# Optimization experiments

Hardware: AMD Instinct MI355X
Metric: run time of the kernel (lower is better)

Reference implementation:

```python
import jax, jax.numpy as jnp
import numpy as np

LN_EPS = 1e-6          # flax nn.LayerNorm default
ATTN_EPS = 1e-9        # numerical_stabilizer default


def ln_points(x, scale, bias):
    """flax LayerNorm(reduction_axes=-2): stats over points axis, affine over feature axis."""
    mu = jnp.mean(x, axis=-2, keepdims=True)
    var = jnp.mean(jnp.square(x), axis=-2, keepdims=True) - jnp.square(mu)
    return (x - mu) * jax.lax.rsqrt(var + LN_EPS) * scale + bias


def self_attention_layer(x, wq_i, bq_i, wk_i, bk_i, wv_i, bv_i, wo_i, bo_i, ls_i, lb_i):
    # 1x1 convs == pointwise linears
    q = x @ wq_i + bq_i                                  # [B,N,C]
    k = x @ wk_i + bk_i
    v = x @ wv_i + bv_i
    attn = jnp.einsum('bmc,bnc->bmn', q, k)              # [B,M,N]
    attn = jax.nn.softmax(attn, axis=-1)
    # extra offset-attention renorm: divide by column sums (axis=1)
    attn = attn / (ATTN_EPS + jnp.sum(attn, axis=1, keepdims=True))
    # einsum '...MN,...NC->...NC' reduces M: scales v by column sums
    col = jnp.sum(attn, axis=1)                          # [B,N]
    out = col[..., None] * v                             # [B,N,C]
    out = out @ wo_i + bo_i
    out = jax.nn.relu(ln_points(out, ls_i, lb_i))
    return out + x


def setup_inputs() -> dict:
    key = jax.random.key(0)
    ks = jax.random.split(key, 16)
    B, N, IN, C, F, L = 2, 4096, 3, 256, 1024, 4
    s_in = 1.0 / np.sqrt(IN)
    s_c = 1.0 / np.sqrt(C)
    s_f = 1.0 / np.sqrt(L * C)
    return {
        'inputs': jax.random.normal(ks[0], (B, N, IN), jnp.float32),
        'w0': jax.random.normal(ks[1], (IN, C), jnp.float32) * s_in,
        'b0': jnp.zeros((C,), jnp.float32),
        'ln0_s': jnp.ones((C,), jnp.float32),
        'ln0_b': jnp.zeros((C,), jnp.float32),
        'w1': jax.random.normal(ks[2], (C, C), jnp.float32) * s_c,
        'b1': jnp.zeros((C,), jnp.float32),
        'ln1_s': jnp.ones((C,), jnp.float32),
        'ln1_b': jnp.zeros((C,), jnp.float32),
        'wq': jax.random.normal(ks[3], (L, C, C), jnp.float32) * s_c,
        'bq': jnp.zeros((L, C), jnp.float32),
        'wk': jax.random.normal(ks[4], (L, C, C), jnp.float32) * s_c,
        'bk': jnp.zeros((L, C), jnp.float32),
        'wv': jax.random.normal(ks[5], (L, C, C), jnp.float32) * s_c,
        'bv': jnp.zeros((L, C), jnp.float32),
        'wo': jax.random.normal(ks[6], (L, C, C), jnp.float32) * s_c,
        'bo': jnp.zeros((L, C), jnp.float32),
        'attn_ln_s': jnp.ones((L, C), jnp.float32),
        'attn_ln_b': jnp.zeros((L, C), jnp.float32),
        'wf': jax.random.normal(ks[7], (L * C, F), jnp.float32) * s_f,
        'bf': jnp.zeros((F,), jnp.float32),
    }


def reference(inputs, w0, b0, ln0_s, ln0_b, w1, b1, ln1_s, ln1_b,
              wq, bq, wk, bk, wv, bv, wo, bo, attn_ln_s, attn_ln_b, wf, bf):
    # pre-conv stack
    out = ln_points(inputs @ w0 + b0, ln0_s, ln0_b)
    out = ln_points(out @ w1 + b1, ln1_s, ln1_b)
    # attention stack (4 structurally identical layers, concatenated)
    attn_outs = []
    for i in range(wq.shape[0]):
        out = self_attention_layer(out, wq[i], bq[i], wk[i], bk[i],
                                   wv[i], bv[i], wo[i], bo[i],
                                   attn_ln_s[i], attn_ln_b[i])
        attn_outs.append(out)
    out = jnp.concatenate(attn_outs, axis=-1)            # [B,N,4C]
    out = out @ wf + bf                                  # [B,N,F]
    return out
```

## Files before the change

### kernel.cpp

```cpp
#include <hip/hip_runtime.h>

#define BB 2
#define NN 4096
#define CC 256
#define FF 1024
#define NLAYER 4
#define RR (BB*NN)
#define SPL 16
#define QKLD (3*CC)
#define NEG_BIG (-1e30f)
#define LOG2E 1.44269504f

typedef _Float16 h16;
typedef __attribute__((ext_vector_type(8))) _Float16 half8;
typedef __attribute__((ext_vector_type(4))) float f32x4;
typedef __attribute__((ext_vector_type(16))) float f32x16;

__device__ __forceinline__ void gload16(const h16* g, h16* l) {
    __builtin_amdgcn_global_load_lds((const __attribute__((address_space(1))) void*)g,
                                     (__attribute__((address_space(3))) void*)l, 16, 0, 0);
}

template<int ROWS>
__device__ __forceinline__ void stage_rows(const h16* __restrict__ src, int ld,
    int row0, int c0, h16* lds, int tid)
{
    int w = tid >> 6;
    #pragma unroll
    for (int t = 0; t < ROWS/32; ++t) {
        int slot = t*256 + tid;
        int row = slot >> 3;
        int pp  = slot & 7;
        int piece = pp ^ (row & 7);
        gload16(src + (size_t)(row0 + row)*ld + c0 + piece*8,
                lds + (t*256 + w*64)*8);
    }
}

__device__ __forceinline__ half8 frag_ld(const h16* lds, int row, int pl) {
    return *(const half8*)(lds + row*64 + ((pl ^ (row & 7))*8));
}

__global__ __launch_bounds__(256) void pct_wtrans(const float* __restrict__ W,
    h16* __restrict__ WT, int K, int N, int dstride, float scale)
{
    __shared__ h16 t[32][33];
    const float* Wl = W + (size_t)blockIdx.z*K*N;
    h16* WTl = WT + (size_t)blockIdx.z*dstride;
    int k0 = blockIdx.x*32, n0 = blockIdx.y*32;
    int tx = threadIdx.x & 31, ty = threadIdx.x >> 5;
    #pragma unroll
    for (int i = ty; i < 32; i += 8)
        t[i][tx] = (h16)(Wl[(size_t)(k0+i)*N + n0 + tx] * scale);
    __syncthreads();
    #pragma unroll
    for (int i = ty; i < 32; i += 8)
        WTl[(size_t)(n0+i)*K + k0 + tx] = t[tx][i];
}

__global__ __launch_bounds__(256) void pct_wtrans_qkv(const float* __restrict__ wq,
    const float* __restrict__ wk, const float* __restrict__ wv, h16* __restrict__ WT)
{
    __shared__ h16 t[32][33];
    int z = blockIdx.z;
    int which = z >> 2, layer = z & 3;
    const float* Wl = (which == 0 ? wq : which == 1 ? wk : wv) + (size_t)layer*CC*CC;
    h16* WTl = WT + (size_t)layer*QKLD*CC + (size_t)which*CC*CC;
    float scale = (which == 0) ? LOG2E : 1.0f;
    int k0 = blockIdx.x*32, n0 = blockIdx.y*32;
    int tx = threadIdx.x & 31, ty = threadIdx.x >> 5;
    #pragma unroll
    for (int i = ty; i < 32; i += 8)
        t[i][tx] = (h16)(Wl[(size_t)(k0+i)*CC + n0 + tx] * scale);
    __syncthreads();
    #pragma unroll
    for (int i = ty; i < 32; i += 8)
        WTl[(size_t)(n0+i)*CC + k0 + tx] = t[tx][i];
}

__global__ __launch_bounds__(256) void pct_bias3(const float* __restrict__ bq,
    const float* __restrict__ bk, const float* __restrict__ bv, float* __restrict__ o)
{
    int l = blockIdx.x, c = threadIdx.x;
    o[l*QKLD + c]        = bq[l*CC + c] * LOG2E;
    o[l*QKLD + CC + c]   = bk[l*CC + c];
    o[l*QKLD + 2*CC + c] = bv[l*CC + c];
}

__global__ __launch_bounds__(256) void pct_embed(const float* __restrict__ inp,
    const float* __restrict__ w0, const float* __restrict__ b0,
    h16* __restrict__ out, float* __restrict__ sums)
{
    int c = threadIdx.x;
    int r0 = blockIdx.x * 64;
    float wa = w0[c], wb = w0[CC+c], wcv = w0[2*CC+c], bb = b0[c];
    float s1 = 0.f, s2 = 0.f;
    #pragma unroll 4
    for (int i = 0; i < 64; ++i) {
        int r = r0 + i;
        float y = bb + inp[r*3+0]*wa + inp[r*3+1]*wb + inp[r*3+2]*wcv;
        h16 hy = (h16)y;
        out[(size_t)r*CC + c] = hy;
        float yf = (float)hy;
        s1 += yf; s2 += yf*yf;
    }
    int b = r0 >> 12;
    atomicAdd(&sums[((size_t)b*CC + c)*2 + 0], s1);
    atomicAdd(&sums[((size_t)b*CC + c)*2 + 1], s2);
}

__global__ __launch_bounds__(256) void pct_lnapply(const h16* __restrict__ x, int ldx,
    const float* __restrict__ sums, const float* __restrict__ scale, const float* __restrict__ bias,
    const h16* __restrict__ res, int ldr, h16* __restrict__ out, int ldo,
    int do_relu)
{
    int r = blockIdx.x*8 + (threadIdx.x >> 5);
    int cg = (threadIdx.x & 31) * 8;
    int b = r / NN;
    half8 xv = *(const half8*)(x + (size_t)r*ldx + cg);
    half8 rv;
    if (res) rv = *(const half8*)(res + (size_t)r*ldr + cg);
    half8 ov;
    #pragma unroll
    for (int j = 0; j < 8; ++j) {
        int c = cg + j;
        float s1 = sums[(b*CC + c)*2], s2 = sums[(b*CC + c)*2 + 1];
        float mu  = s1 * (1.f/NN);
        float var = s2 * (1.f/NN) - mu*mu;
        float rstd = rsqrtf(var + 1e-6f);
        float y = ((float)xv[j] - mu) * rstd * scale[c] + bias[c];
        if (do_relu) y = fmaxf(y, 0.f);
        if (res) y += (float)rv[j];
        ov[j] = (h16)y;
    }
    *(half8*)(out + (size_t)r*ldo + cg) = ov;
}

template<int BN, bool OUT_F32, bool CSTAT>
__global__ __launch_bounds__(256) void pct_gemm_f16(
    const h16* __restrict__ A, int lda,
    const h16* __restrict__ WT, const float* __restrict__ bias,
    void* __restrict__ outp, int ldo, int K, const float* __restrict__ rowS,
    float* __restrict__ csums)
{
    constexpr int BJ = BN/2;
    constexpr int NF = BJ/16;
    __shared__ __align__(16) h16 Asm[128*64];
    __shared__ __align__(16) h16 Bsm[BN*64];
    const int tid = threadIdx.x;
    const int lane = tid & 63, w = tid >> 6;
    const int ln = lane & 15, lq = lane >> 4;
    const int wr = w >> 1, wc = w & 1;
    const int m0 = blockIdx.x*128, n0 = blockIdx.y*BN;
    f32x4 acc[4][NF];
    #pragma unroll
    for (int i = 0; i < 4; ++i)
        #pragma unroll
        for (int j = 0; j < NF; ++j) acc[i][j] = (f32x4){0.f,0.f,0.f,0.f};
    for (int k0 = 0; k0 < K; k0 += 64) {
        stage_rows<128>(A, lda, m0, k0, Asm, tid);
        stage_rows<BN>(WT, K, n0, k0, Bsm, tid);
        __syncthreads();
        #pragma unroll
        for (int kk = 0; kk < 2; ++kk) {
            half8 af[4], bfr[NF];
            #pragma unroll
            for (int i = 0; i < 4; ++i) af[i] = frag_ld(Asm, wr*64 + i*16 + ln, kk*4 + lq);
            #pragma unroll
            for (int j = 0; j < NF; ++j) bfr[j] = frag_ld(Bsm, wc*BJ + j*16 + ln, kk*4 + lq);
            #pragma unroll
            for (int i = 0; i < 4; ++i)
                #pragma unroll
                for (int j = 0; j < NF; ++j)
                    acc[i][j] = __builtin_amdgcn_mfma_f32_16x16x32_f16(af[i], bfr[j], acc[i][j], 0, 0, 0);
        }
        __syncthreads();
    }
    float cs1[NF], cs2[NF];
    #pragma unroll
    for (int j = 0; j < NF; ++j) {
        int col = n0 + wc*BJ + j*16 + ln;
        float bv = bias[col];
        float s1 = 0.f, s2 = 0.f;
        #pragma unroll
        for (int i = 0; i < 4; ++i) {
            #pragma unroll
            for (int r = 0; r < 4; ++r) {
                int row = m0 + wr*64 + i*16 + lq*4 + r;
                float sc = 1.f;
                if (rowS) { float s = rowS[row]; sc = s / (1e-9f + s); }
                float v = acc[i][j][r] * sc + bv;
                if (OUT_F32) ((float*)outp)[(size_t)row*ldo + col] = v;
                else ((h16*)outp)[(size_t)row*ldo + col] = (h16)v;
                if (CSTAT) { s1 += v; s2 += v*v; }
            }
        }
        cs1[j] = s1; cs2[j] = s2;
    }
    if constexpr (CSTAT) {
        __shared__ float cred[2][2][BJ][2];
        #pragma unroll
        for (int j = 0; j < NF; ++j) {
            float s1 = cs1[j], s2 = cs2[j];
            s1 += __shfl_down(s1, 16); s1 += __shfl_down(s1, 32);
            s2 += __shfl_down(s2, 16); s2 += __shfl_down(s2, 32);
            if (lane < 16) {
                cred[wr][wc][j*16 + lane][0] = s1;
                cred[wr][wc][j*16 + lane][1] = s2;
            }
        }
        __syncthreads();
        if (tid < 2*BN) {
            int c = tid >> 1, st = tid & 1;
            int wcc = c >> 5, ci = c & 31;
            float v = cred[0][wcc][ci][st] + cred[1][wcc][ci][st];
            int b = m0 >> 12;
            atomicAdd(&csums[((size_t)b*CC + n0 + c)*2 + st], v);
        }
    }
}

__global__ __launch_bounds__(256) void attn_rowstats(const h16* __restrict__ QKV,
    float2* __restrict__ part)
{
    __shared__ __align__(16) h16 Ks[2][128*64];
    const int b = blockIdx.x, mt = blockIdx.y, sp = blockIdx.z;
    const int tid = threadIdx.x;
    const int lane = tid & 63, w = tid >> 6;
    const int ln2 = lane & 31, h = lane >> 5;
    const h16* qb = QKV + (size_t)b*NN*QKLD;
    const h16* kb = qb + CC;
    const int m0 = mt*128;
    const h16* qrow = qb + (size_t)(m0 + w*32 + ln2)*QKLD + h*8;
    half8 qreg[16];
    #pragma unroll
    for (int i = 0; i < 16; ++i) qreg[i] = *(const half8*)(qrow + i*16);

    const int nbeg = sp*(NN/SPL);
    const int NT = (NN/SPL)/128;
    float rm = NEG_BIG, rs = 0.f;

    stage_rows<128>(kb, QKLD, nbeg, 0, Ks[0], tid);
    int id = 0;
    for (int t = 0; t < NT; ++t) {
        f32x16 acc[4];
        #pragma unroll
        for (int j = 0; j < 4; ++j) acc[j] = (f32x16)(0.f);
        #pragma unroll
        for (int c = 0; c < 4; ++c, ++id) {
            __syncthreads();
            if (id + 1 < NT*4)
                stage_rows<128>(kb, QKLD, nbeg + ((id+1) >> 2)*128, ((id+1) & 3)*64,
                                Ks[(id+1) & 1], tid);
            const h16* buf = Ks[id & 1];
            #pragma unroll
            for (int kk = 0; kk < 4; ++kk) {
                half8 bq = qreg[c*4 + kk];
                #pragma unroll
                for (int j = 0; j < 4; ++j) {
                    half8 af = frag_ld(buf, j*32 + ln2, kk*2 + h);
                    acc[j] = __builtin_amdgcn_mfma_f32_32x32x16_f16(af, bq, acc[j], 0, 0, 0);
                }
            }
        }
        float tm = NEG_BIG;
        #pragma unroll
        for (int j = 0; j < 4; ++j)
            #pragma unroll
            for (int g = 0; g < 16; g += 2)
                tm = fmaxf(tm, fmaxf(acc[j][g], acc[j][g+1]));
        if (tm > rm) { rs *= exp2f(rm - tm); rm = tm; }
        float s = 0.f;
        #pragma unroll
        for (int j = 0; j < 4; ++j)
            #pragma unroll
            for (int g = 0; g < 16; ++g)
                s += exp2f(acc[j][g] - rm);
        rs += s;
    }
    float mo = __shfl_xor(rm, 32, 64);
    float so = __shfl_xor(rs, 32, 64);
    float mn = fmaxf(rm, mo);
    float sm = rs*exp2f(rm - mn) + so*exp2f(mo - mn);
    if (lane < 32) {
        int m = m0 + w*32 + ln2;
        part[((size_t)b*NN + m)*SPL + sp] = make_float2(mn, sm);
    }
}

__global__ __launch_bounds__(256) void pct_rowcomb(const float2* __restrict__ part,
    float2* __restrict__ rstat)
{
    int idx = blockIdx.x*256 + threadIdx.x;
    const float2* p = part + (size_t)idx*SPL;
    float m = NEG_BIG;
    #pragma unroll
    for (int s = 0; s < SPL; ++s) m = fmaxf(m, p[s].x);
    float sum = 0.f;
    #pragma unroll
    for (int s = 0; s < SPL; ++s) sum += p[s].y * exp2f(p[s].x - m);
    rstat[idx] = make_float2(m, 1.0f / sum);
}

__global__ __launch_bounds__(256) void attn_colsums(const h16* __restrict__ QKV,
    const float2* __restrict__ rstat, float* __restrict__ S)
{
    __shared__ __align__(16) h16 Qs[2][128*64];
    const int b = blockIdx.x, nt = blockIdx.y, sp = blockIdx.z;
    const int tid = threadIdx.x;
    const int lane = tid & 63, w = tid >> 6;
    const int ln2 = lane & 31, h = lane >> 5;
    const h16* qb = QKV + (size_t)b*NN*QKLD;
    const h16* kb = qb + CC;
    const float2* rst = rstat + (size_t)b*NN;
    const int n0 = nt*128;
    const h16* krow = kb + (size_t)(n0 + w*32 + ln2)*QKLD + h*8;
    half8 kreg[16];
    #pragma unroll
    for (int i = 0; i < 16; ++i) kreg[i] = *(const half8*)(krow + i*16);

    const int mbeg = sp*(NN/SPL);
    const int NT = (NN/SPL)/128;
    float cs = 0.f;

    stage_rows<128>(qb, QKLD, mbeg, 0, Qs[0], tid);
    int id = 0;
    for (int t = 0; t < NT; ++t) {
        f32x16 acc[4];
        #pragma unroll
        for (int j = 0; j < 4; ++j) acc[j] = (f32x16)(0.f);
        #pragma unroll
        for (int c = 0; c < 4; ++c, ++id) {
            __syncthreads();
            if (id + 1 < NT*4)
                stage_rows<128>(qb, QKLD, mbeg + ((id+1) >> 2)*128, ((id+1) & 3)*64,
                                Qs[(id+1) & 1], tid);
            const h16* buf = Qs[id & 1];
            #pragma unroll
            for (int kk = 0; kk < 4; ++kk) {
                half8 bk = kreg[c*4 + kk];
                #pragma unroll
                for (int j = 0; j < 4; ++j) {
                    half8 af = frag_ld(buf, j*32 + ln2, kk*2 + h);
                    acc[j] = __builtin_amdgcn_mfma_f32_32x32x16_f16(af, bk, acc[j], 0, 0, 0);
                }
            }
        }
        int mt0 = mbeg + t*128;
        #pragma unroll
        for (int j = 0; j < 4; ++j) {
            #pragma unroll
            for (int g = 0; g < 16; ++g) {
                int m = mt0 + j*32 + (g & 3) + 8*(g >> 2) + 4*h;
                float2 st = rst[m];
                cs += exp2f(acc[j][g] - st.x) * st.y;
            }
        }
    }
    cs += __shfl_xor(cs, 32, 64);
    if (lane < 32) {
        int n = n0 + w*32 + ln2;
        atomicAdd(&S[(size_t)b*NN + n], cs);
    }
}

extern "C" void kernel_launch(void* const* d_in, const int* in_sizes, int n_in,
                              void* d_out, int out_size, void* d_ws, size_t ws_size,
                              hipStream_t stream)
{
    const float* inp  = (const float*)d_in[0];
    const float* w0   = (const float*)d_in[1];
    const float* b0   = (const float*)d_in[2];
    const float* ln0s = (const float*)d_in[3];
    const float* ln0b = (const float*)d_in[4];
    const float* w1   = (const float*)d_in[5];
    const float* b1   = (const float*)d_in[6];
    const float* ln1s = (const float*)d_in[7];
    const float* ln1b = (const float*)d_in[8];
    const float* wq   = (const float*)d_in[9];
    const float* bq   = (const float*)d_in[10];
    const float* wk   = (const float*)d_in[11];
    const float* bk   = (const float*)d_in[12];
    const float* wv   = (const float*)d_in[13];
    const float* bv   = (const float*)d_in[14];
    const float* wo   = (const float*)d_in[15];
    const float* bo   = (const float*)d_in[16];
    const float* alns = (const float*)d_in[17];
    const float* alnb = (const float*)d_in[18];
    const float* wf   = (const float*)d_in[19];
    const float* bfb  = (const float*)d_in[20];
    float* out = (float*)d_out;

    char* p = (char*)d_ws;
    auto alloc = [&](size_t bytes) { char* r = p; p += (bytes + 255) & ~255ULL; return r; };
    h16* t0    = (h16*)alloc((size_t)RR*CC*2);
    h16* t1    = (h16*)alloc((size_t)RR*CC*2);
    h16* t2    = (h16*)alloc((size_t)RR*CC*2);
    h16* x1    = (h16*)alloc((size_t)RR*CC*2);
    h16* qkv   = (h16*)alloc((size_t)RR*QKLD*2);
    h16* oh    = (h16*)alloc((size_t)RR*CC*2);
    h16* xcat  = (h16*)alloc((size_t)RR*FF*2);
    h16* w1T   = (h16*)alloc((size_t)CC*CC*2);
    h16* wqkvT = (h16*)alloc((size_t)NLAYER*QKLD*CC*2);
    h16* woT   = (h16*)alloc((size_t)NLAYER*CC*CC*2);
    h16* wfT   = (h16*)alloc((size_t)FF*FF*2);
    float* bqkv  = (float*)alloc((size_t)NLAYER*QKLD*4);
    float2* part  = (float2*)alloc((size_t)RR*SPL*8);
    float2* rstat = (float2*)alloc((size_t)RR*8);
    float* Ssum  = (float*)alloc((size_t)NLAYER*RR*4);
    float* lns   = (float*)alloc((size_t)6*BB*CC*2*4);

    dim3 blk(256);

    hipMemsetAsync(Ssum, 0, (size_t)((char*)(lns + 6*BB*CC*2) - (char*)Ssum), stream);

    pct_wtrans<<<dim3(CC/32, CC/32, 1), blk, 0, stream>>>(w1, w1T, CC, CC, CC*CC, 1.f);
    pct_wtrans_qkv<<<dim3(CC/32, CC/32, 3*NLAYER), blk, 0, stream>>>(wq, wk, wv, wqkvT);
    pct_wtrans<<<dim3(CC/32, CC/32, NLAYER), blk, 0, stream>>>(wo, woT, CC, CC, CC*CC, 1.f);
    pct_wtrans<<<dim3(FF/32, FF/32, 1), blk, 0, stream>>>(wf, wfT, FF, FF, FF*FF, 1.f);
    pct_bias3<<<NLAYER, blk, 0, stream>>>(bq, bk, bv, bqkv);

    pct_embed<<<RR/64, blk, 0, stream>>>(inp, w0, b0, t0, lns + 0*BB*CC*2);
    pct_lnapply<<<RR/8, blk, 0, stream>>>(t0, CC, lns + 0*BB*CC*2, ln0s, ln0b, nullptr, 0, t1, CC, 0);
    pct_gemm_f16<64,false,true><<<dim3(RR/128, CC/64), blk, 0, stream>>>(
        t1, CC, w1T, b1, t2, CC, CC, nullptr, lns + 1*BB*CC*2);
    pct_lnapply<<<RR/8, blk, 0, stream>>>(t2, CC, lns + 1*BB*CC*2, ln1s, ln1b, nullptr, 0, x1, CC, 0);

    const h16* xin = x1; int ldx = CC;
    for (int i = 0; i < NLAYER; ++i) {
        pct_gemm_f16<64,false,false><<<dim3(RR/128, QKLD/64), blk, 0, stream>>>(
            xin, ldx, wqkvT + (size_t)i*QKLD*CC, bqkv + i*QKLD, qkv, QKLD, CC, nullptr, nullptr);

        attn_rowstats<<<dim3(BB, NN/128, SPL), blk, 0, stream>>>(qkv, part);
        pct_rowcomb<<<RR/256, blk, 0, stream>>>(part, rstat);
        attn_colsums<<<dim3(BB, NN/128, SPL), blk, 0, stream>>>(qkv, rstat, Ssum + (size_t)i*RR);

        pct_gemm_f16<64,false,true><<<dim3(RR/128, CC/64), blk, 0, stream>>>(
            qkv + 2*CC, QKLD, woT + (size_t)i*CC*CC, bo + i*CC, oh, CC, CC,
            Ssum + (size_t)i*RR, lns + (2+i)*BB*CC*2);

        pct_lnapply<<<RR/8, blk, 0, stream>>>(oh, CC, lns + (2+i)*BB*CC*2, alns + i*CC, alnb + i*CC,
                                              xin, ldx, xcat + i*CC, FF, 1);
        xin = xcat + i*CC; ldx = FF;
    }

    pct_gemm_f16<128,true,false><<<dim3(RR/128, FF/128), blk, 0, stream>>>(
        xcat, FF, wfT, bfb, out, FF, FF, nullptr, nullptr);
}
```

Measured before the change: 554.8 us.

## Triple-buffer attention K/Q staging and fold row-stat combine into colsums

Both attention kernels now use a three-slot LDS ring that prefetches two chunks ahead. The full __syncthreads is replaced by an explicit vmcnt wait plus s_barrier, and MFMA sections are bracketed with s_setprio so loads overlap more with math. The separate row-combine kernel is removed: each colsums block recomputes the max and inverse-sum for its 256 rows from the partials into shared memory. This saves a launch and a global round trip, at the cost of redundant combine work across the 32 n-tiles and higher LDS use, which may lower occupancy.

Measured after the change: 498.6 us. 1.11x faster.

```diff
diff --git a/kernel.cpp b/kernel.cpp
--- a/kernel.cpp
+++ b/kernel.cpp
@@ -15,6 +15,9 @@
 typedef __attribute__((ext_vector_type(8))) _Float16 half8;
 typedef __attribute__((ext_vector_type(4))) float f32x4;
 typedef __attribute__((ext_vector_type(16))) float f32x16;
+
+#define WAITVM4 asm volatile("s_waitcnt vmcnt(4)" ::: "memory")
+#define WAITVM0 asm volatile("s_waitcnt vmcnt(0)" ::: "memory")
 
 __device__ __forceinline__ void gload16(const h16* g, h16* l) {
     __builtin_amdgcn_global_load_lds((const __attribute__((address_space(1))) void*)g,
@@ -223,7 +226,7 @@
 __global__ __launch_bounds__(256) void attn_rowstats(const h16* __restrict__ QKV,
     float2* __restrict__ part)
 {
-    __shared__ __align__(16) h16 Ks[2][128*64];
+    __shared__ __align__(16) h16 Ks[3*128*64];
     const int b = blockIdx.x, mt = blockIdx.y, sp = blockIdx.z;
     const int tid = threadIdx.x;
     const int lane = tid & 63, w = tid >> 6;
@@ -237,22 +240,27 @@
     for (int i = 0; i < 16; ++i) qreg[i] = *(const half8*)(qrow + i*16);
 
     const int nbeg = sp*(NN/SPL);
-    const int NT = (NN/SPL)/128;
+    constexpr int NT = (NN/SPL)/128;
+    constexpr int NCH = NT*4;
     float rm = NEG_BIG, rs = 0.f;
 
-    stage_rows<128>(kb, QKLD, nbeg, 0, Ks[0], tid);
+    stage_rows<128>(kb, QKLD, nbeg, 0, Ks, tid);
+    stage_rows<128>(kb, QKLD, nbeg, 64, Ks + 8192, tid);
     int id = 0;
+    #pragma unroll
     for (int t = 0; t < NT; ++t) {
         f32x16 acc[4];
         #pragma unroll
         for (int j = 0; j < 4; ++j) acc[j] = (f32x16)(0.f);
         #pragma unroll
         for (int c = 0; c < 4; ++c, ++id) {
-            __syncthreads();
-            if (id + 1 < NT*4)
-                stage_rows<128>(kb, QKLD, nbeg + ((id+1) >> 2)*128, ((id+1) & 3)*64,
-                                Ks[(id+1) & 1], tid);
-            const h16* buf = Ks[id & 1];
+            if (id == NCH-1) { WAITVM0; } else { WAITVM4; }
+            __builtin_amdgcn_s_barrier();
+            if (id + 2 < NCH)
+                stage_rows<128>(kb, QKLD, nbeg + ((id+2) >> 2)*128, ((id+2) & 3)*64,
+                                Ks + ((id+2) % 3)*8192, tid);
+            const h16* buf = Ks + (id % 3)*8192;
+            __builtin_amdgcn_s_setprio(1);
             #pragma unroll
             for (int kk = 0; kk < 4; ++kk) {
                 half8 bq = qreg[c*4 + kk];
@@ -262,6 +270,7 @@
                     acc[j] = __builtin_amdgcn_mfma_f32_32x32x16_f16(af, bq, acc[j], 0, 0, 0);
                 }
             }
+            __builtin_amdgcn_s_setprio(0);
         }
         float tm = NEG_BIG;
         #pragma unroll
@@ -288,54 +297,58 @@
     }
 }
 
-__global__ __launch_bounds__(256) void pct_rowcomb(const float2* __restrict__ part,
-    float2* __restrict__ rstat)
-{
-    int idx = blockIdx.x*256 + threadIdx.x;
-    const float2* p = part + (size_t)idx*SPL;
-    float m = NEG_BIG;
-    #pragma unroll
-    for (int s = 0; s < SPL; ++s) m = fmaxf(m, p[s].x);
-    float sum = 0.f;
-    #pragma unroll
-    for (int s = 0; s < SPL; ++s) sum += p[s].y * exp2f(p[s].x - m);
-    rstat[idx] = make_float2(m, 1.0f / sum);
-}
-
 __global__ __launch_bounds__(256) void attn_colsums(const h16* __restrict__ QKV,
-    const float2* __restrict__ rstat, float* __restrict__ S)
-{
-    __shared__ __align__(16) h16 Qs[2][128*64];
+    const float2* __restrict__ part, float* __restrict__ S)
+{
+    __shared__ __align__(16) h16 Qs[3*128*64];
+    __shared__ float2 rst_s[256];
     const int b = blockIdx.x, nt = blockIdx.y, sp = blockIdx.z;
     const int tid = threadIdx.x;
     const int lane = tid & 63, w = tid >> 6;
     const int ln2 = lane & 31, h = lane >> 5;
     const h16* qb = QKV + (size_t)b*NN*QKLD;
     const h16* kb = qb + CC;
-    const float2* rst = rstat + (size_t)b*NN;
     const int n0 = nt*128;
+    const int mbeg = sp*(NN/SPL);
+
+    {
+        const float2* pp = part + ((size_t)b*NN + mbeg + tid)*SPL;
+        float m = NEG_BIG;
+        #pragma unroll
+        for (int s = 0; s < SPL; ++s) m = fmaxf(m, pp[s].x);
+        float sum = 0.f;
+        #pragma unroll
+        for (int s = 0; s < SPL; ++s) sum += pp[s].y * exp2f(pp[s].x - m);
+        rst_s[tid] = make_float2(m, 1.0f / sum);
+    }
+    __syncthreads();
+
     const h16* krow = kb + (size_t)(n0 + w*32 + ln2)*QKLD + h*8;
     half8 kreg[16];
     #pragma unroll
     for (int i = 0; i < 16; ++i) kreg[i] = *(const half8*)(krow + i*16);
 
-    const int mbeg = sp*(NN/SPL);
-    const int NT = (NN/SPL)/128;
+    constexpr int NT = (NN/SPL)/128;
+    constexpr int NCH = NT*4;
     float cs = 0.f;
 
-    stage_rows<128>(qb, QKLD, mbeg, 0, Qs[0], tid);
+    stage_rows<128>(qb, QKLD, mbeg, 0, Qs, tid);
+    stage_rows<128>(qb, QKLD, mbeg, 64, Qs + 8192, tid);
     int id = 0;
+    #pragma unroll
     for (int t = 0; t < NT; ++t) {
         f32x16 acc[4];
         #pragma unroll
         for (int j = 0; j < 4; ++j) acc[j] = (f32x16)(0.f);
         #pragma unroll
         for (int c = 0; c < 4; ++c, ++id) {
-            __syncthreads();
-            if (id + 1 < NT*4)
-                stage_rows<128>(qb, QKLD, mbeg + ((id+1) >> 2)*128, ((id+1) & 3)*64,
-                                Qs[(id+1) & 1], tid);
-            const h16* buf = Qs[id & 1];
+            if (id == NCH-1) { WAITVM0; } else { WAITVM4; }
+            __builtin_amdgcn_s_barrier();
+            if (id + 2 < NCH)
+                stage_rows<128>(qb, QKLD, mbeg + ((id+2) >> 2)*128, ((id+2) & 3)*64,
+                                Qs + ((id+2) % 3)*8192, tid);
+            const h16* buf = Qs + (id % 3)*8192;
+            __builtin_amdgcn_s_setprio(1);
             #pragma unroll
             for (int kk = 0; kk < 4; ++kk) {
                 half8 bk = kreg[c*4 + kk];
@@ -345,14 +358,15 @@
                     acc[j] = __builtin_amdgcn_mfma_f32_32x32x16_f16(af, bk, acc[j], 0, 0, 0);
                 }
             }
-        }
-        int mt0 = mbeg + t*128;
+            __builtin_amdgcn_s_setprio(0);
+        }
+        int mt0 = t*128;
         #pragma unroll
         for (int j = 0; j < 4; ++j) {
             #pragma unroll
             for (int g = 0; g < 16; ++g) {
-                int m = mt0 + j*32 + (g & 3) + 8*(g >> 2) + 4*h;
-                float2 st = rst[m];
+                int mloc = mt0 + j*32 + (g & 3) + 8*(g >> 2) + 4*h;
+                float2 st = rst_s[mloc];
                 cs += exp2f(acc[j][g] - st.x) * st.y;
             }
         }
@@ -406,7 +420,6 @@
     h16* wfT   = (h16*)alloc((size_t)FF*FF*2);
     float* bqkv  = (float*)alloc((size_t)NLAYER*QKLD*4);
     float2* part  = (float2*)alloc((size_t)RR*SPL*8);
-    float2* rstat = (float2*)alloc((size_t)RR*8);
     float* Ssum  = (float*)alloc((size_t)NLAYER*RR*4);
     float* lns   = (float*)alloc((size_t)6*BB*CC*2*4);
 
@@ -432,8 +445,7 @@
             xin, ldx, wqkvT + (size_t)i*QKLD*CC, bqkv + i*QKLD, qkv, QKLD, CC, nullptr, nullptr);
 
         attn_rowstats<<<dim3(BB, NN/128, SPL), blk, 0, stream>>>(qkv, part);
-        pct_rowcomb<<<RR/256, blk, 0, stream>>>(part, rstat);
-        attn_colsums<<<dim3(BB, NN/128, SPL), blk, 0, stream>>>(qkv, rstat, Ssum + (size_t)i*RR);
+        attn_colsums<<<dim3(BB, NN/128, SPL), blk, 0, stream>>>(qkv, part, Ssum + (size_t)i*RR);
 
         pct_gemm_f16<64,false,true><<<dim3(RR/128, CC/64), blk, 0, stream>>>(
             qkv + 2*CC, QKLD, woT + (size_t)i*CC*CC, bo + i*CC, oh, CC, CC,
```
